# Kernel optimization log

Measured on AMD Instinct MI355X. Metric: run time of the kernel, lower is better.

The kernel has to match this reference:

```python
import jax, jax.numpy as jnp
import numpy as np

D = 1024
D_H = 64

def setup_inputs() -> dict:
    key = jax.random.key(0)
    kx, kq, kk, kv = jax.random.split(key, 4)
    B, T = 4, 4096
    x = jax.random.normal(kx, (B, T, D), dtype=jnp.float32)
    # nn.Linear(d, d_H, bias=False) weights, stored as [d, d_H] (already transposed)
    s = 1.0 / np.sqrt(D)
    Wq = jax.random.uniform(kq, (D, D_H), dtype=jnp.float32, minval=-s, maxval=s)
    Wk = jax.random.uniform(kk, (D, D_H), dtype=jnp.float32, minval=-s, maxval=s)
    Wv = jax.random.uniform(kv, (D, D_H), dtype=jnp.float32, minval=-s, maxval=s)
    return {"x": x, "Wq": Wq, "Wk": Wk, "Wv": Wv}

def reference(x, Wq, Wk, Wv):
    B, T, d = x.shape
    Q = jnp.einsum('btd,dh->bth', x, Wq)
    K = jnp.einsum('btd,dh->bth', x, Wk)
    V = jnp.einsum('btd,dh->bth', x, Wv)
    # NOTE: original scales by self.d ** -0.5 (model dim), not d_H
    scores = jnp.einsum('bqh,bkh->bqk', Q, K) * (d ** -0.5)
    causal = jnp.tril(jnp.ones((T, T), dtype=bool))  # [T, T]
    scores = jnp.where(causal, scores, -jnp.inf)
    attn = jax.nn.softmax(scores, axis=-1)
    return jnp.einsum('bqk,bkh->bqh', attn, V)
```

## Files before the change

kernel.cpp:

```cpp
#include <hip/hip_runtime.h>
#include <hip/hip_bf16.h>

#define D_MODEL 1024
#define D_HEAD  64
#define T_SEQ   4096
#define NB      4
#define NROWS   (NB * T_SEQ)
#define SPLIT   8

typedef float f32x4 __attribute__((ext_vector_type(4)));
typedef __bf16 bf16x8 __attribute__((ext_vector_type(8)));
typedef unsigned short u16;
typedef unsigned u32x2 __attribute__((ext_vector_type(2)));
typedef unsigned u32x4 __attribute__((ext_vector_type(4)));

__device__ inline unsigned pk_bf16(float a, float b) {
    unsigned ua = __builtin_bit_cast(unsigned, a);
    unsigned ub = __builtin_bit_cast(unsigned, b);
    ua = (ua + 0x7FFFu + ((ua >> 16) & 1u)) >> 16;
    ub = (ub + 0x7FFFu + ((ub >> 16) & 1u)) >> 16;
    return ua | (ub << 16);
}
__device__ inline u16 bf16r(float a) {
    unsigned ua = __builtin_bit_cast(unsigned, a);
    return (u16)((ua + 0x7FFFu + ((ua >> 16) & 1u)) >> 16);
}
__device__ inline unsigned cvtpk_bf16(float lo, float hi) {
    unsigned r;
    asm("v_cvt_pk_bf16_f32 %0, %1, %2" : "=v"(r) : "v"(lo), "v"(hi));
    return r;
}

__device__ inline void gload_lds16(const void* g, void* l) {
    __builtin_amdgcn_global_load_lds(
        (const __attribute__((address_space(1))) void*)g,
        (__attribute__((address_space(3))) void*)l, 16, 0, 0);
}

__global__ __launch_bounds__(256) void packw_kernel(
    const float* __restrict__ Wq, const float* __restrict__ Wk,
    const float* __restrict__ Wv, unsigned* __restrict__ Wpk)
{
    const int id = blockIdx.x * 256 + threadIdx.x;
    const int kb = id / 192;
    const int n  = id - kb * 192;
    const int sel = n >> 6, col = n & 63;
    const float* W = sel == 0 ? Wq : (sel == 1 ? Wk : Wv);
    float f[8];
#pragma unroll
    for (int j = 0; j < 8; ++j) f[j] = W[(kb * 8 + j) * 64 + col];
    uint4 o;
    o.x = pk_bf16(f[0], f[1]); o.y = pk_bf16(f[2], f[3]);
    o.z = pk_bf16(f[4], f[5]); o.w = pk_bf16(f[6], f[7]);
    *(uint4*)(Wpk + (size_t)id * 4) = o;
}

__global__ __launch_bounds__(256) void qkv_kernel(
    const float* __restrict__ x, const unsigned* __restrict__ Wpk,
    u16* __restrict__ Qbf, u16* __restrict__ Kbf, u16* __restrict__ Vt)
{
    __shared__ __align__(16) unsigned Xs[2][32 * 68];
    __shared__ __align__(16) u16 Vbuf[64 * 32];

    const int tid  = threadIdx.x;
    const int w    = tid >> 6;
    const int lane = tid & 63;
    const int nl   = lane & 15;
    const int quad = lane >> 4;
    const long row0 = (long)blockIdx.x * 32;

    const int srow = tid >> 5;
    const int scol = (tid & 31) * 4;

    f32x4 acc[2][3] = {};

    float4 nx[4];
#pragma unroll
    for (int p = 0; p < 4; ++p)
        nx[p] = *(const float4*)(x + (row0 + p * 8 + srow) * D_MODEL + scol);

    for (int ch = 0; ch < 8; ++ch) {
        const int buf = ch & 1;
#pragma unroll
        for (int p = 0; p < 4; ++p) {
            uint2 pk2;
            pk2.x = pk_bf16(nx[p].x, nx[p].y);
            pk2.y = pk_bf16(nx[p].z, nx[p].w);
            *(uint2*)&Xs[buf][(p * 8 + srow) * 68 + (scol >> 1)] = pk2;
        }
        __syncthreads();
        if (ch < 7) {
#pragma unroll
            for (int p = 0; p < 4; ++p)
                nx[p] = *(const float4*)(x + (row0 + p * 8 + srow) * D_MODEL
                                           + (ch + 1) * 128 + scol);
        }
#pragma unroll
        for (int kk = 0; kk < 4; ++kk) {
            const bf16x8 a0 = __builtin_bit_cast(bf16x8,
                *(const uint4*)&Xs[buf][nl * 68 + kk * 16 + quad * 4]);
            const bf16x8 a1 = __builtin_bit_cast(bf16x8,
                *(const uint4*)&Xs[buf][(16 + nl) * 68 + kk * 16 + quad * 4]);
            const unsigned* wb = Wpk + (size_t)(ch * 16 + kk * 4 + quad) * 768
                                     + (w * 48 + nl) * 4;
#pragma unroll
            for (int t = 0; t < 3; ++t) {
                const bf16x8 b = __builtin_bit_cast(bf16x8, *(const uint4*)(wb + t * 64));
                acc[0][t] = __builtin_amdgcn_mfma_f32_16x16x32_bf16(a0, b, acc[0][t], 0, 0, 0);
                acc[1][t] = __builtin_amdgcn_mfma_f32_16x16x32_bf16(a1, b, acc[1][t], 0, 0, 0);
            }
        }
    }
    __syncthreads();

    const float QSCALE = 0.04508422f;
#pragma unroll
    for (int t = 0; t < 3; ++t) {
        const int n0c = w * 48 + t * 16;
        const int sel = n0c >> 6;
        const int col = (n0c & 63) + nl;
#pragma unroll
        for (int m = 0; m < 2; ++m) {
            if (sel == 0) {
#pragma unroll
                for (int reg = 0; reg < 4; ++reg)
                    Qbf[(row0 + m * 16 + quad * 4 + reg) * D_HEAD + col] =
                        bf16r(acc[m][t][reg] * QSCALE);
            } else if (sel == 1) {
#pragma unroll
                for (int reg = 0; reg < 4; ++reg)
                    Kbf[(row0 + m * 16 + quad * 4 + reg) * D_HEAD + col] =
                        bf16r(acc[m][t][reg]);
            } else {
                uint2 p2;
                p2.x = pk_bf16(acc[m][t][0], acc[m][t][1]);
                p2.y = pk_bf16(acc[m][t][2], acc[m][t][3]);
                *(uint2*)&Vbuf[col * 32 + m * 16 + quad * 4] = p2;
            }
        }
    }
    __syncthreads();
    {
        const int dim  = tid >> 2;
        const int tseg = (tid & 3) * 8;
        const long bb   = row0 >> 12;
        const int tpos0 = (int)(row0 & 4095);
        const uint4 v = *(const uint4*)&Vbuf[dim * 32 + tseg];
        *(uint4*)&Vt[((bb * 64 + dim) << 12) + tpos0 + tseg] = v;
    }
}

__global__ __launch_bounds__(256, 2) void attn_kernel(
    const u16* __restrict__ Qbf, const u16* __restrict__ Kbf,
    const u16* __restrict__ Vt, u16* __restrict__ Po16, float* __restrict__ Pl)
{
    __shared__ __align__(16) u16 Kls[2][4096];
    __shared__ __align__(16) u16 Pbuf[4][2][16 * 64];

    const int tid   = threadIdx.x;
    const int w     = tid >> 6;
    const int lane  = tid & 63;
    const int nl    = lane & 15;
    const int quad  = lane >> 4;
    const int gid   = blockIdx.x;
    const int b     = gid & 3;
    const int idx   = gid >> 2;
    const int sp    = idx & 7;
    const int pair  = idx >> 3;

    const u16* Kb = Kbf + (size_t)b * T_SEQ * D_HEAD;
    const u16* Vb = Vt  + (size_t)b * D_HEAD * T_SEQ;

    const int qbA = 31 - pair;
    const int qbB = pair;
    const int nA = 2 * qbA + 2;
    const int nB = 2 * qbB + 2;
    const int cntA = (nA - sp + 7) >> 3;
    const int ktB0 = sp + SPLIT * cntA - nA;
    const int cntB = (ktB0 < nB) ? ((nB - ktB0 + 7) >> 3) : 0;

    const int swz   = ((lane & 7) ^ ((lane >> 3) & 7)) * 8;
    const int stgk  = ((lane >> 3) << 6) + swz;
    const int offh0 = nl * 64 + ((quad ^ (nl & 7)) << 3);
    const int offh1 = nl * 64 + (((quad + 4) ^ (nl & 7)) << 3);
    const int pwsub = ((quad & 1) << 2);
    const int pg0   = (quad >> 1);

#define STAGE(cur_, kt_) do {                                                        \
    const int _s0 = (kt_) << 6;                                                      \
    _Pragma("unroll") for (int jj = 0; jj < 2; ++jj) {                               \
        const int j = w * 2 + jj;                                                    \
        gload_lds16(Kb + (size_t)(_s0 + 8 * j) * 64 + stgk, &Kls[cur_][j * 512]);    \
    }                                                                                \
} while (0)

#define COMPUTEKV(cur_, kt_) do {                                                    \
    const int _k0 = (kt_) << 6;                                                      \
    uint4 buf[4][2];                                                                 \
    _Pragma("unroll") for (int t = 0; t < 4; ++t) {                                  \
        buf[t][0] = *(const uint4*)&Kls[cur_][t * 1024 + offh0];                     \
        buf[t][1] = *(const uint4*)&Kls[cur_][t * 1024 + offh1];                     \
    }                                                                                \
    f32x4 S[2][4];                                                                   \
    _Pragma("unroll") for (int m = 0; m < 2; ++m)                                    \
    _Pragma("unroll") for (int t = 0; t < 4; ++t) {                                  \
        f32x4 z = {};                                                                \
        z = __builtin_amdgcn_mfma_f32_16x16x32_bf16(                                 \
                __builtin_bit_cast(bf16x8, buf[t][0]), qf[m][0], z, 0, 0, 0);        \
        S[m][t] = __builtin_amdgcn_mfma_f32_16x16x32_bf16(                           \
                __builtin_bit_cast(bf16x8, buf[t][1]), qf[m][1], z, 0, 0, 0);        \
    }                                                                                \
    uint4 vbuf[4][2];          \
    _Pragma("unroll") for (int t = 0; t < 4; ++t) {                                  \
        const u16* vp = Vb + (size_t)(t * 16 + nl) * T_SEQ + _k0 + quad * 8;         \
        vbuf[t][0] = *(const uint4*)vp;                                              \
        vbuf[t][1] = *(const uint4*)(vp + 32);                                       \
    }                                                                                \
    _Pragma("unroll") for (int m = 0; m < 2; ++m) {                                  \
        const int _q = wq0 + m * 16 + nl;                     \
        if (_k0 + 63 > wq0 + m * 16) {                                               \
            _Pragma("unroll") for (int t = 0; t < 4; ++t)                            \
            _Pragma("unroll") for (int reg = 0; reg < 4; ++reg)                      \
                if (_k0 + t * 16 + quad * 4 + reg > _q)                              \
                    S[m][t][reg] = -INFINITY;                                        \
        }                                                                            \
        _Pragma("unroll") for (int t = 0; t < 4; ++t)                                \
        _Pragma("unroll") for (int reg = 0; reg < 4; ++reg)                          \
            S[m][t][reg] = exp2f(S[m][t][reg]);                                      \
        float _lm = 0.f;                                                             \
        _Pragma("unroll") for (int t = 0; t < 4; ++t)                                \
            _lm += (S[m][t][0] + S[m][t][1]) + (S[m][t][2] + S[m][t][3]);            \
        l[m] += _lm;                                                                 \
        u16* pb = Pbuf[w][m];                                                        \
        _Pragma("unroll") for (int t = 0; t < 4; ++t) {                              \
            u32x2 pw;                                                                \
            pw[0] = cvtpk_bf16(S[m][t][0], S[m][t][1]);                              \
            pw[1] = cvtpk_bf16(S[m][t][2], S[m][t][3]);                              \
            *(u32x2*)&pb[nl * 64 + (((2 * t + pg0) ^ (nl & 7)) << 3) + pwsub] = pw;  \
        }                                                                            \
    }                                                                                \
    _Pragma("unroll") for (int m = 0; m < 2; ++m) {                                  \
        const u16* pb = Pbuf[w][m];                                                  \
        const bf16x8 pf0 = __builtin_bit_cast(bf16x8,                                \
            *(const uint4*)&pb[nl * 64 + ((quad ^ (nl & 7)) * 8)]);                  \
        const bf16x8 pf1 = __builtin_bit_cast(bf16x8,                                \
            *(const uint4*)&pb[nl * 64 + (((4 + quad) ^ (nl & 7)) * 8)]);            \
        _Pragma("unroll") for (int t = 0; t < 4; ++t) {                              \
            Ot[m][t] = __builtin_amdgcn_mfma_f32_16x16x32_bf16(pf0,                  \
                        __builtin_bit_cast(bf16x8, vbuf[t][0]), Ot[m][t], 0, 0, 0);  \
            Ot[m][t] = __builtin_amdgcn_mfma_f32_16x16x32_bf16(pf1,                  \
                        __builtin_bit_cast(bf16x8, vbuf[t][1]), Ot[m][t], 0, 0, 0);  \
        }                                                                            \
    }                                                                                \
} while (0)

    auto runTile = [&](const int qb, const int kt0, const int cnt) {
        const int wq0 = qb * 128 + w * 32;

        bf16x8 qf[2][2];
#pragma unroll
        for (int m = 0; m < 2; ++m) {
            const u16* qp = Qbf + ((size_t)b * T_SEQ + wq0 + m * 16 + nl) * D_HEAD + quad * 8;
            qf[m][0] = __builtin_bit_cast(bf16x8, *(const uint4*)qp);
            qf[m][1] = __builtin_bit_cast(bf16x8, *(const uint4*)(qp + 32));
        }

        f32x4 Ot[2][4] = {};
        float l[2] = {0.f, 0.f};

        int kt = kt0;
        if (cnt > 0) STAGE(0, kt);
        __syncthreads();
        for (int i = 0; i < cnt; ++i, kt += SPLIT) {
            if (i + 1 < cnt) STAGE((i + 1) & 1, kt + SPLIT);
            COMPUTEKV(i & 1, kt);
            __syncthreads();
        }

#pragma unroll
        for (int m = 0; m < 2; ++m) {
            float s = l[m];
            s += __shfl_xor(s, 16);
            s += __shfl_xor(s, 32);
            const int strip = qb * 8 + w * 2 + m;
            const int bs = b * 256 + strip;
            u16* po = Po16 + ((size_t)sp * 1024 + bs) * 1024;
#pragma unroll
            for (int t = 0; t < 4; ++t) {
                u32x2 p2;
                p2[0] = pk_bf16(Ot[m][t][0], Ot[m][t][1]);
                p2[1] = pk_bf16(Ot[m][t][2], Ot[m][t][3]);
                __builtin_nontemporal_store(p2, (u32x2*)&po[(t * 16 + nl) * 16 + quad * 4]);
            }
            if (lane < 16) {
                const size_t gr = (size_t)b * T_SEQ + qb * 128 + w * 32 + m * 16;
                __builtin_nontemporal_store(s, &Pl[(size_t)sp * NROWS + gr + nl]);
            }
        }
    };

    runTile(qbA, sp,   cntA);
    runTile(qbB, ktB0, cntB);

#undef STAGE
#undef COMPUTEKV
}

__global__ __launch_bounds__(256) void reduce_kernel(
    const u16* __restrict__ Po16, const float* __restrict__ Pl,
    float* __restrict__ O)
{
    __shared__ float part[4][16][64];
    __shared__ float lsum[4][16];
    __shared__ float linv[16];
    const int tid = threadIdx.x;
    const int w   = tid >> 6;
    const int c   = tid & 63;
    const int bs  = blockIdx.x;
    const int b   = bs >> 8, strip = bs & 255;
    const size_t gr = (size_t)b * T_SEQ + strip * 16;

    float v[16] = {};
    float ls = 0.f;
#pragma unroll
    for (int i = 0; i < 2; ++i) {
        const int sp = w + i * 4;
        const u16* p = Po16 + ((size_t)sp * 1024 + bs) * 1024 + c * 16;
        const u32x4 x0 = __builtin_nontemporal_load((const u32x4*)p);
        const u32x4 x1 = __builtin_nontemporal_load((const u32x4*)p + 1);
        const unsigned uu[8] = {x0[0], x0[1], x0[2], x0[3], x1[0], x1[1], x1[2], x1[3]};
#pragma unroll
        for (int j = 0; j < 8; ++j) {
            v[2*j]   += __builtin_bit_cast(float, uu[j] << 16);
            v[2*j+1] += __builtin_bit_cast(float, uu[j] & 0xFFFF0000u);
        }
        if (c < 16) ls += Pl[(size_t)sp * NROWS + gr + c];
    }
#pragma unroll
    for (int r = 0; r < 16; ++r) part[w][r][c] = v[r];
    if (c < 16) lsum[w][c] = ls;
    __syncthreads();
    if (tid < 16)
        linv[tid] = 1.0f / (lsum[0][tid] + lsum[1][tid] + lsum[2][tid] + lsum[3][tid]);
    __syncthreads();
#pragma unroll
    for (int j = 0; j < 4; ++j) {
        const int r = w + j * 4;
        const float s = (part[0][r][c] + part[1][r][c]) + (part[2][r][c] + part[3][r][c]);
        O[(gr + r) * D_HEAD + c] = s * linv[r];
    }
}

extern "C" void kernel_launch(void* const* d_in, const int* in_sizes, int n_in,
                              void* d_out, int out_size, void* d_ws, size_t ws_size,
                              hipStream_t stream) {
    const float* x  = (const float*)d_in[0];
    const float* Wq = (const float*)d_in[1];
    const float* Wk = (const float*)d_in[2];
    const float* Wv = (const float*)d_in[3];
    float* out = (float*)d_out;

    const size_t rows = NROWS;
    u16* Qbf = (u16*)d_ws;
    u16* Kbf = Qbf + rows * D_HEAD;
    u16* Vt  = Kbf + rows * D_HEAD;
    unsigned* Wpk = (unsigned*)(Vt + rows * D_HEAD);
    u16* Po16 = (u16*)(Wpk + 128 * 192 * 4);
    float* Pl = (float*)(Po16 + (size_t)SPLIT * rows * D_HEAD);

    hipLaunchKernelGGL(packw_kernel, dim3(96), dim3(256), 0, stream,
                       Wq, Wk, Wv, Wpk);
    hipLaunchKernelGGL(qkv_kernel, dim3(rows / 32), dim3(256), 0, stream,
                       x, Wpk, Qbf, Kbf, Vt);
    hipLaunchKernelGGL(attn_kernel, dim3(512), dim3(256), 0, stream,
                       Qbf, Kbf, Vt, Po16, Pl);
    hipLaunchKernelGGL(reduce_kernel, dim3(NB * 256), dim3(64 * 4), 0, stream,
                       Po16, Pl, out);
}
```

Measured before the change: 139.3 us.

## Stage x via direct global-to-LDS loads with swizzle, convert to bf16 at read

The QKV projection kernel now stages fp32 x tiles straight into shared memory with direct global-to-LDS loads, instead of loading into registers, converting to bf16 and storing. The tile uses an XOR swizzle to avoid bank conflicts, and the bf16 conversion moves to the point where MFMA operands are read from LDS. This is meant to cut register staging and VGPR pressure and to overlap the next chunk's load with the current compute. In exchange, LDS use doubles because fp32 is stored, and each tile's conversion work is repeated per read.

```diff
diff --git a/kernel.cpp b/kernel.cpp
--- a/kernel.cpp
+++ b/kernel.cpp
@@ -59,7 +59,7 @@
     const float* __restrict__ x, const unsigned* __restrict__ Wpk,
     u16* __restrict__ Qbf, u16* __restrict__ Kbf, u16* __restrict__ Vt)
 {
-    __shared__ __align__(16) unsigned Xs[2][32 * 68];
+    __shared__ __align__(16) float Xs[2][32 * 128];
     __shared__ __align__(16) u16 Vbuf[64 * 32];
 
     const int tid  = threadIdx.x;
@@ -69,38 +69,40 @@
     const int quad = lane >> 4;
     const long row0 = (long)blockIdx.x * 32;
 
-    const int srow = tid >> 5;
-    const int scol = (tid & 31) * 4;
+    const float* xb = x + row0 * D_MODEL;
+
+    const int rbase = w * 2 + (lane >> 5);
+    const int sgs   = (lane & 31) ^ (rbase & 7);
+
+#define XSTAGE(buf_, ch_) do {                                                       \
+    _Pragma("unroll") for (int p = 0; p < 4; ++p)                                    \
+        gload_lds16(xb + (size_t)(p * 8 + rbase) * D_MODEL + (ch_) * 128 + sgs * 4,  \
+                    &Xs[buf_][p * 1024 + w * 256]);                                  \
+} while (0)
 
     f32x4 acc[2][3] = {};
-
-    float4 nx[4];
-#pragma unroll
-    for (int p = 0; p < 4; ++p)
-        nx[p] = *(const float4*)(x + (row0 + p * 8 + srow) * D_MODEL + scol);
+    const int nlx = nl & 7;
+
+    XSTAGE(0, 0);
+    __syncthreads();
 
     for (int ch = 0; ch < 8; ++ch) {
         const int buf = ch & 1;
-#pragma unroll
-        for (int p = 0; p < 4; ++p) {
-            uint2 pk2;
-            pk2.x = pk_bf16(nx[p].x, nx[p].y);
-            pk2.y = pk_bf16(nx[p].z, nx[p].w);
-            *(uint2*)&Xs[buf][(p * 8 + srow) * 68 + (scol >> 1)] = pk2;
-        }
-        __syncthreads();
-        if (ch < 7) {
-#pragma unroll
-            for (int p = 0; p < 4; ++p)
-                nx[p] = *(const float4*)(x + (row0 + p * 8 + srow) * D_MODEL
-                                           + (ch + 1) * 128 + scol);
-        }
+        if (ch < 7) XSTAGE(buf ^ 1, ch + 1);
 #pragma unroll
         for (int kk = 0; kk < 4; ++kk) {
-            const bf16x8 a0 = __builtin_bit_cast(bf16x8,
-                *(const uint4*)&Xs[buf][nl * 68 + kk * 16 + quad * 4]);
-            const bf16x8 a1 = __builtin_bit_cast(bf16x8,
-                *(const uint4*)&Xs[buf][(16 + nl) * 68 + kk * 16 + quad * 4]);
+            const int s0 = kk * 8 + quad * 2;
+            const f32x4 fA0 = *(const f32x4*)&Xs[buf][nl * 128 + ((s0) ^ nlx) * 4];
+            const f32x4 fA1 = *(const f32x4*)&Xs[buf][nl * 128 + ((s0 + 1) ^ nlx) * 4];
+            const f32x4 fB0 = *(const f32x4*)&Xs[buf][(16 + nl) * 128 + ((s0) ^ nlx) * 4];
+            const f32x4 fB1 = *(const f32x4*)&Xs[buf][(16 + nl) * 128 + ((s0 + 1) ^ nlx) * 4];
+            u32x4 ua, ub;
+            ua[0] = cvtpk_bf16(fA0[0], fA0[1]); ua[1] = cvtpk_bf16(fA0[2], fA0[3]);
+            ua[2] = cvtpk_bf16(fA1[0], fA1[1]); ua[3] = cvtpk_bf16(fA1[2], fA1[3]);
+            ub[0] = cvtpk_bf16(fB0[0], fB0[1]); ub[1] = cvtpk_bf16(fB0[2], fB0[3]);
+            ub[2] = cvtpk_bf16(fB1[0], fB1[1]); ub[3] = cvtpk_bf16(fB1[2], fB1[3]);
+            const bf16x8 a0 = __builtin_bit_cast(bf16x8, ua);
+            const bf16x8 a1 = __builtin_bit_cast(bf16x8, ub);
             const unsigned* wb = Wpk + (size_t)(ch * 16 + kk * 4 + quad) * 768
                                      + (w * 48 + nl) * 4;
 #pragma unroll
@@ -110,8 +112,8 @@
                 acc[1][t] = __builtin_amdgcn_mfma_f32_16x16x32_bf16(a1, b, acc[1][t], 0, 0, 0);
             }
         }
-    }
-    __syncthreads();
+        __syncthreads();
+    }
 
     const float QSCALE = 0.04508422f;
 #pragma unroll
```

New measurement: 136.4 us (median of 2 runs). 1.02x faster.
